# Performance work log

Hardware: AMD Instinct MI355X
Metric: run time of the kernel (lower is better)

Reference implementation:

```python
import jax, jax.numpy as jnp
import numpy as np

H = 16          # num_heads
EPS = 1e-5      # torch LayerNorm default eps


def setup_inputs() -> dict:
    key = jax.random.key(0)
    ks = jax.random.split(key, 12)
    B, S, D = 4, 2048, 1024
    sc = 1.0 / np.sqrt(D)
    return {
        "queries": jax.random.normal(ks[0], (B, S, D), jnp.float32),
        "keys": jax.random.normal(ks[1], (B, S, D), jnp.float32),
        "values": jax.random.normal(ks[2], (B, S, D), jnp.float32),
        "attention_mask": jax.random.randint(ks[3], (B, S), 0, 2, jnp.int32),
        "Wq": jax.random.normal(ks[4], (D, D), jnp.float32) * sc,
        "bq": jnp.zeros((D,), jnp.float32),
        "Wk": jax.random.normal(ks[5], (D, D), jnp.float32) * sc,
        "bk": jnp.zeros((D,), jnp.float32),
        "Wv": jax.random.normal(ks[6], (D, D), jnp.float32) * sc,
        "bv": jnp.zeros((D,), jnp.float32),
        "gamma": jnp.ones((D,), jnp.float32),
        "beta": jnp.zeros((D,), jnp.float32),
    }


def reference(queries, keys, values, attention_mask, Wq, bq, Wk, bk, Wv, bv, gamma, beta):
    B, S, D = queries.shape
    dh = D // H

    # QKV projections with ReLU epilogue (nn.Sequential(Linear, ReLU))
    q = jax.nn.relu(jnp.einsum("bsd,de->bse", queries, Wq) + bq)
    k = jax.nn.relu(jnp.einsum("bsd,de->bse", keys, Wk) + bk)
    v = jax.nn.relu(jnp.einsum("bsd,de->bse", values, Wv) + bv)

    # chunk along last dim + stack at dim=1  ==  [B,S,H,dh] -> [B,H,S,dh]
    q_ = q.reshape(B, S, H, dh).transpose(0, 2, 1, 3)
    k_ = k.reshape(B, S, H, dh).transpose(0, 2, 1, 3)
    v_ = v.reshape(B, S, H, dh).transpose(0, 2, 1, 3)

    # scaled dot-product scores [B,H,S,S]
    scores = jnp.einsum("bhqd,bhkd->bhqk", q_, k_) / jnp.sqrt(jnp.float32(dh))

    # mask[b,h,i,j] = attention_mask[b,i]; masked positions set to 1e-9
    # (faithful to torch.masked_fill(value=1e-09) in the original)
    m = attention_mask[:, None, :, None].astype(bool)  # [B,1,S,1]
    scores = jnp.where(m, scores, jnp.float32(1e-9))

    a = jax.nn.softmax(scores, axis=-1)
    o = jnp.einsum("bhqk,bhkd->bhqd", a, v_)          # [B,H,S,dh]
    o = o.transpose(0, 2, 1, 3).reshape(B, S, D)

    # residual + LayerNorm
    x = o + queries
    mu = jnp.mean(x, axis=-1, keepdims=True)
    var = jnp.mean(jnp.square(x - mu), axis=-1, keepdims=True)
    return (x - mu) * jax.lax.rsqrt(var + EPS) * gamma + beta
```

## Files before the change

kernel.cpp:

```cpp
#include <hip/hip_runtime.h>
#include <hip/hip_bf16.h>
#include <stdint.h>

typedef __bf16 bf16x8 __attribute__((ext_vector_type(8)));
typedef float f32x4 __attribute__((ext_vector_type(4)));
typedef float f32x16 __attribute__((ext_vector_type(16)));
typedef unsigned short ushort8v __attribute__((ext_vector_type(8)));
typedef unsigned short ushort4v __attribute__((ext_vector_type(4)));
typedef uint32_t uint2v __attribute__((ext_vector_type(2)));

#define MFMA16(a, b, c) __builtin_amdgcn_mfma_f32_16x16x32_bf16(a, b, c, 0, 0, 0)
#define MFMA32(a, b, c) __builtin_amdgcn_mfma_f32_32x32x16_bf16(a, b, c, 0, 0, 0)

#define GLOAD_LDS16(g, l)                                                        \
    __builtin_amdgcn_global_load_lds(                                            \
        (const __attribute__((address_space(1))) uint32_t*)(g),                  \
        (__attribute__((address_space(3))) uint32_t*)(l), 16, 0, 0)

__device__ __forceinline__ unsigned short f2bf_u(float f) {
    union { float f; uint32_t u; } cv; cv.f = f;
    uint32_t u = cv.u;
    uint32_t r = (u + 0x7FFFu + ((u >> 16) & 1u)) >> 16;
    return (unsigned short)r;
}

__device__ __forceinline__ uint32_t pkbf(float a, float b) {
    union { __hip_bfloat162 h; uint32_t u; } cv;
    cv.h = __float22bfloat162_rn(make_float2(a, b));
    return cv.u;
}

__device__ __forceinline__ float fexp2(float x) { return __builtin_amdgcn_exp2f(x); }

__global__ __launch_bounds__(256) void wt_cast(const float* __restrict__ W0,
                                               const float* __restrict__ W1,
                                               const float* __restrict__ W2,
                                               unsigned short* __restrict__ T0,
                                               unsigned short* __restrict__ T1,
                                               unsigned short* __restrict__ T2) {
    const int z = blockIdx.z;
    const float* W = z == 0 ? W0 : (z == 1 ? W1 : W2);
    unsigned short* Wt = z == 0 ? T0 : (z == 1 ? T1 : T2);
    __shared__ float t[32][33];
    const int tx = threadIdx.x & 31, ty = threadIdx.x >> 5;
    const int n0 = blockIdx.x * 32, k0 = blockIdx.y * 32;
#pragma unroll
    for (int i = 0; i < 4; i++) {
        int r = i * 8 + ty;
        t[r][tx] = W[(size_t)(k0 + r) * 1024 + n0 + tx];
    }
    __syncthreads();
#pragma unroll
    for (int i = 0; i < 4; i++) {
        int r = i * 8 + ty;
        Wt[(size_t)(n0 + r) * 1024 + k0 + tx] = f2bf_u(t[tx][r]);
    }
}

__global__ __launch_bounds__(256) void qkv_gemm2(
    const float* __restrict__ Aq, const float* __restrict__ Ak, const float* __restrict__ Av,
    const unsigned short* __restrict__ Wq, const unsigned short* __restrict__ Wk,
    const unsigned short* __restrict__ Wv,
    const float* __restrict__ biasq, const float* __restrict__ biask,
    const float* __restrict__ biasv,
    unsigned short* __restrict__ outq, unsigned short* __restrict__ outk,
    unsigned short* __restrict__ outv) {
    __shared__ __align__(16) unsigned short aS[2][128 * 32];
    __shared__ __align__(16) unsigned short wS[2][128 * 32];
    const int id = blockIdx.x;
    const int xcd = id & 7;
    const int local = id >> 3;
    const int z = local >> 6;
    const int l2i = local & 63;
    const int m0 = (xcd * 8 + (l2i >> 3)) * 128;
    const int n0 = (l2i & 7) * 128;

    const float* A = z == 0 ? Aq : (z == 1 ? Ak : Av);
    const unsigned short* Wt = z == 0 ? Wq : (z == 1 ? Wk : Wv);
    const float* bias = z == 0 ? biasq : (z == 1 ? biask : biasv);
    unsigned short* out = z == 0 ? outq : (z == 1 ? outk : outv);
    const bool vt = (z == 2);

    const int tid = threadIdx.x;
    const int lane = tid & 63, wave = tid >> 6;
    const int rrow = lane & 15, rgrp = lane >> 4;
    const int wm = wave >> 1, wn = wave & 1;

    const int wrow0 = tid >> 2, wc0 = tid & 3;
    const int wrow1 = (tid + 256) >> 2;
    const int arow_f = wm * 64 + rrow;
    const int brow_f = wn * 64 + rrow;

    f32x4 acc[4][4];
#pragma unroll
    for (int i = 0; i < 4; i++)
#pragma unroll
        for (int j = 0; j < 4; j++) acc[i][j] = (f32x4)0.0f;

    auto STAGE_W = [&](int k0, int bufi) {
        const char* src = (const char*)Wt;
        char* dst = (char*)&wS[bufi][0] + wave * 1024;
        GLOAD_LDS16(src + ((size_t)(n0 + wrow0) * 1024 + k0 + wc0 * 8) * 2, dst);
        GLOAD_LDS16(src + ((size_t)(n0 + wrow1) * 1024 + k0 + wc0 * 8) * 2, dst + 4096);
    };
    auto LOAD_A = [&](int k0, float4* r) {
#pragma unroll
        for (int i = 0; i < 4; i++) {
            const int g = i * 256 + tid, row = g >> 3, qc = g & 7;
            r[i] = *reinterpret_cast<const float4*>(A + (size_t)(m0 + row) * 1024 + k0 + qc * 4);
        }
    };
    auto WRITE_A = [&](const float4* r, int bufi) {
#pragma unroll
        for (int i = 0; i < 4; i++) {
            const int g = i * 256 + tid, row = g >> 3, qc = g & 7;
            uint2v w;
            w[0] = pkbf(r[i].x, r[i].y);
            w[1] = pkbf(r[i].z, r[i].w);
            *reinterpret_cast<uint2v*>((char*)&aS[bufi][0] + row * 64 + qc * 8) = w;
        }
    };

    {
        float4 a0[4];
        STAGE_W(0, 0);
        LOAD_A(0, a0);
        WRITE_A(a0, 0);
    }
    __syncthreads();

    for (int ks = 0; ks < 32; ks++) {
        const int cur = ks & 1;
        float4 anx[4];
        if (ks < 31) {
            STAGE_W((ks + 1) * 32, cur ^ 1);
            LOAD_A((ks + 1) * 32, anx);
        }

        bf16x8 af[4], bfr[4];
#pragma unroll
        for (int mi = 0; mi < 4; mi++)
            af[mi] = *reinterpret_cast<const bf16x8*>(
                (const char*)&aS[cur][0] + (arow_f + mi * 16) * 64 + rgrp * 16);
#pragma unroll
        for (int ni = 0; ni < 4; ni++)
            bfr[ni] = *reinterpret_cast<const bf16x8*>(
                (const char*)&wS[cur][0] + (brow_f + ni * 16) * 64 + rgrp * 16);
        __builtin_amdgcn_s_setprio(1);
#pragma unroll
        for (int mi = 0; mi < 4; mi++)
#pragma unroll
            for (int ni = 0; ni < 4; ni++)
                acc[mi][ni] = MFMA16(af[mi], bfr[ni], acc[mi][ni]);
        __builtin_amdgcn_s_setprio(0);

        if (ks < 31) WRITE_A(anx, cur ^ 1);
        __syncthreads();
    }

#pragma unroll
    for (int mi = 0; mi < 4; mi++) {
#pragma unroll
        for (int ni = 0; ni < 4; ni++) {
            const int n = n0 + wn * 64 + ni * 16 + rrow;
            const float bv = bias[n];
            const int h = n >> 6, d = n & 63;
            const int mbase = m0 + wm * 64 + mi * 16 + rgrp * 4;
            const int b = mbase >> 11, s = mbase & 2047;
            if (vt) {
                ushort4v pv;
#pragma unroll
                for (int jr = 0; jr < 4; jr++)
                    pv[jr] = f2bf_u(fmaxf(acc[mi][ni][jr] + bv, 0.0f));
                *reinterpret_cast<ushort4v*>(out + ((size_t)((b * 16 + h) * 64 + d)) * 2048 + s) = pv;
            } else {
#pragma unroll
                for (int jr = 0; jr < 4; jr++)
                    out[((size_t)((b * 16 + h) * 2048 + (s + jr))) * 64 + d] =
                        f2bf_u(fmaxf(acc[mi][ni][jr] + bv, 0.0f));
            }
        }
    }
}

__global__ __launch_bounds__(256, 4) void flash_attn(const unsigned short* __restrict__ Qg,
                                                     const unsigned short* __restrict__ Kg,
                                                     const unsigned short* __restrict__ Vt,
                                                     const int* __restrict__ mask,
                                                     float* __restrict__ O) {
    __shared__ __align__(16) unsigned short ldsK[2][64 * 64];
    __shared__ __align__(16) unsigned short ldsV[2][64 * 64];
    const int tid = threadIdx.x;
    const int lane = tid & 63, wave = tid >> 6;
    const int c = lane & 31, hi = lane >> 5;
    const int bid = blockIdx.x;
    const int swzb = (bid & 7) * 128 + (bid >> 3);
    const int gid = swzb * 4 + wave;
    const int bh = gid >> 6;
    const int q0 = (gid & 63) * 32;
    const int b = bh >> 4, h = bh & 15;
    const size_t base = (size_t)bh * (2048 * 64);
    const unsigned short* Qb = Qg + base;
    const unsigned short* Kb = Kg + base;
    const unsigned short* Vb = Vt + base;

    const int srow = lane >> 3;
    const int schunk = (lane & 7) ^ srow;
    int offL[4], offH[4];
#pragma unroll
    for (int ds = 0; ds < 4; ds++) {
        offL[ds] = c * 128 + ((((ds << 1) + hi) ^ (c & 7)) << 4);
        offH[ds] = offL[ds] + 32 * 128;
    }

    bf16x8 qf[4];
#pragma unroll
    for (int ds = 0; ds < 4; ds++)
        qf[ds] = *reinterpret_cast<const bf16x8*>(Qb + (size_t)(q0 + c) * 64 + ds * 16 + hi * 8);

    const int mk = mask[b * 2048 + q0 + c];
    const float sc = mk ? 0.1803368801f : 0.0f;

    union { uint32_t u[4]; bf16x8 v; } onesf;
#pragma unroll
    for (int i = 0; i < 4; i++) onesf.u[i] = 0x3F803F80u;

    f32x16 lacc = (f32x16)0.0f;
    f32x16 oacc0 = (f32x16)0.0f, oacc1 = (f32x16)0.0f;

    auto STAGE = [&](int kt, int bufi) {
        const char* ktile = (const char*)Kb + (size_t)kt * 8192;
        const char* vtile = (const char*)Vb + (size_t)kt * 128;
        char* kdst = (char*)&ldsK[bufi][0] + wave * 2048;
        char* vdst = (char*)&ldsV[bufi][0] + wave * 2048;
#pragma unroll
        for (int i = 0; i < 2; i++) {
            const int row = wave * 16 + i * 8 + srow;
            GLOAD_LDS16(ktile + row * 128 + schunk * 16, kdst + i * 1024);
            GLOAD_LDS16(vtile + (size_t)row * 4096 + schunk * 16, vdst + i * 1024);
        }
    };

    STAGE(0, 0);
    __syncthreads();

    for (int kt = 0; kt < 32; kt++) {
        const int cur = kt & 1;
        if (kt < 31) STAGE(kt + 1, cur ^ 1);
        const char* kbuf = (const char*)&ldsK[cur][0];
        const char* vbuf = (const char*)&ldsV[cur][0];

        f32x16 sacc0 = (f32x16)0.0f, sacc1 = (f32x16)0.0f;
        __builtin_amdgcn_s_setprio(1);
#pragma unroll
        for (int ds = 0; ds < 4; ds++) {
            bf16x8 k0 = *reinterpret_cast<const bf16x8*>(kbuf + offL[ds]);
            bf16x8 k1 = *reinterpret_cast<const bf16x8*>(kbuf + offH[ds]);
            sacc0 = MFMA32(k0, qf[ds], sacc0);
            sacc1 = MFMA32(k1, qf[ds], sacc1);
        }
        __builtin_amdgcn_s_setprio(0);

#pragma unroll
        for (int j = 0; j < 16; j++) {
            sacc0[j] = fexp2(sacc0[j] * sc);
            sacc1[j] = fexp2(sacc1[j] * sc);
        }

        {
            uint32_t w0[8];
#pragma unroll
            for (int i = 0; i < 8; i++) w0[i] = pkbf(sacc0[2 * i], sacc0[2 * i + 1]);
            uint32_t s00 = __shfl_xor(hi ? w0[0] : w0[2], 32, 64);
            uint32_t s01 = __shfl_xor(hi ? w0[1] : w0[3], 32, 64);
            uint32_t s02 = __shfl_xor(hi ? w0[4] : w0[6], 32, 64);
            uint32_t s03 = __shfl_xor(hi ? w0[5] : w0[7], 32, 64);
            union { uint32_t u[4]; bf16x8 v; } pa[2];
            if (hi == 0) {
                pa[0].u[0] = w0[0]; pa[0].u[1] = w0[1]; pa[0].u[2] = s00; pa[0].u[3] = s01;
                pa[1].u[0] = w0[4]; pa[1].u[1] = w0[5]; pa[1].u[2] = s02; pa[1].u[3] = s03;
            } else {
                pa[0].u[0] = s00; pa[0].u[1] = s01; pa[0].u[2] = w0[2]; pa[0].u[3] = w0[3];
                pa[1].u[0] = s02; pa[1].u[1] = s03; pa[1].u[2] = w0[6]; pa[1].u[3] = w0[7];
            }
            __builtin_amdgcn_s_setprio(1);
#pragma unroll
            for (int ks = 0; ks < 2; ks++) {
                bf16x8 v0 = *reinterpret_cast<const bf16x8*>(vbuf + offL[ks]);
                bf16x8 v1 = *reinterpret_cast<const bf16x8*>(vbuf + offH[ks]);
                lacc = MFMA32(pa[ks].v, onesf.v, lacc);
                oacc0 = MFMA32(pa[ks].v, v0, oacc0);
                oacc1 = MFMA32(pa[ks].v, v1, oacc1);
            }
            __builtin_amdgcn_s_setprio(0);
        }
        {
            uint32_t w1[8];
#pragma unroll
            for (int i = 0; i < 8; i++) w1[i] = pkbf(sacc1[2 * i], sacc1[2 * i + 1]);
            uint32_t s10 = __shfl_xor(hi ? w1[0] : w1[2], 32, 64);
            uint32_t s11 = __shfl_xor(hi ? w1[1] : w1[3], 32, 64);
            uint32_t s12 = __shfl_xor(hi ? w1[4] : w1[6], 32, 64);
            uint32_t s13 = __shfl_xor(hi ? w1[5] : w1[7], 32, 64);
            union { uint32_t u[4]; bf16x8 v; } pa[2];
            if (hi == 0) {
                pa[0].u[0] = w1[0]; pa[0].u[1] = w1[1]; pa[0].u[2] = s10; pa[0].u[3] = s11;
                pa[1].u[0] = w1[4]; pa[1].u[1] = w1[5]; pa[1].u[2] = s12; pa[1].u[3] = s13;
            } else {
                pa[0].u[0] = s10; pa[0].u[1] = s11; pa[0].u[2] = w1[2]; pa[0].u[3] = w1[3];
                pa[1].u[0] = s12; pa[1].u[1] = s13; pa[1].u[2] = w1[6]; pa[1].u[3] = w1[7];
            }
            __builtin_amdgcn_s_setprio(1);
#pragma unroll
            for (int ks = 0; ks < 2; ks++) {
                bf16x8 v0 = *reinterpret_cast<const bf16x8*>(vbuf + offL[2 + ks]);
                bf16x8 v1 = *reinterpret_cast<const bf16x8*>(vbuf + offH[2 + ks]);
                lacc = MFMA32(pa[ks].v, onesf.v, lacc);
                oacc0 = MFMA32(pa[ks].v, v0, oacc0);
                oacc1 = MFMA32(pa[ks].v, v1, oacc1);
            }
            __builtin_amdgcn_s_setprio(0);
        }

        __syncthreads();
    }

#pragma unroll
    for (int reg = 0; reg < 16; reg++) {
        const int rr = (reg & 3) + 8 * (reg >> 2) + 4 * hi;
        const float ir = 1.0f / lacc[reg];
        const size_t rowoff = (size_t)(b * 2048 + q0 + rr) * 1024 + h * 64 + c;
        O[rowoff]      = oacc0[reg] * ir;
        O[rowoff + 32] = oacc1[reg] * ir;
    }
}

__global__ __launch_bounds__(256) void resid_ln(const float* __restrict__ O,
                                                const float* __restrict__ Qin,
                                                const float* __restrict__ gamma,
                                                const float* __restrict__ beta,
                                                float* __restrict__ out) {
    __shared__ float red[4];
    const int row = blockIdx.x, tid = threadIdx.x;
    const size_t base = (size_t)row * 1024 + tid * 4;
    float4 o4 = *reinterpret_cast<const float4*>(O + base);
    float4 q4 = *reinterpret_cast<const float4*>(Qin + base);
    float x0 = o4.x + q4.x, x1 = o4.y + q4.y, x2 = o4.z + q4.z, x3 = o4.w + q4.w;

    float s = x0 + x1 + x2 + x3;
#pragma unroll
    for (int off = 32; off >= 1; off >>= 1) s += __shfl_xor(s, off, 64);
    const int w = tid >> 6;
    if ((tid & 63) == 0) red[w] = s;
    __syncthreads();
    const float mean = (red[0] + red[1] + red[2] + red[3]) * (1.0f / 1024.0f);
    __syncthreads();

    const float d0 = x0 - mean, d1 = x1 - mean, d2 = x2 - mean, d3 = x3 - mean;
    float vs = d0 * d0 + d1 * d1 + d2 * d2 + d3 * d3;
#pragma unroll
    for (int off = 32; off >= 1; off >>= 1) vs += __shfl_xor(vs, off, 64);
    if ((tid & 63) == 0) red[w] = vs;
    __syncthreads();
    const float var = (red[0] + red[1] + red[2] + red[3]) * (1.0f / 1024.0f);
    const float rstd = rsqrtf(var + 1e-5f);

    float4 g = *reinterpret_cast<const float4*>(gamma + tid * 4);
    float4 be = *reinterpret_cast<const float4*>(beta + tid * 4);
    float4 r;
    r.x = d0 * rstd * g.x + be.x;
    r.y = d1 * rstd * g.y + be.y;
    r.z = d2 * rstd * g.z + be.z;
    r.w = d3 * rstd * g.w + be.w;
    *reinterpret_cast<float4*>(out + base) = r;
}

extern "C" void kernel_launch(void* const* d_in, const int* in_sizes, int n_in,
                              void* d_out, int out_size, void* d_ws, size_t ws_size,
                              hipStream_t stream) {
    const float* q_in = (const float*)d_in[0];
    const float* k_in = (const float*)d_in[1];
    const float* v_in = (const float*)d_in[2];
    const int* mask = (const int*)d_in[3];
    const float* Wq = (const float*)d_in[4];
    const float* bq = (const float*)d_in[5];
    const float* Wk = (const float*)d_in[6];
    const float* bk = (const float*)d_in[7];
    const float* Wv = (const float*)d_in[8];
    const float* bv = (const float*)d_in[9];
    const float* gamma = (const float*)d_in[10];
    const float* beta = (const float*)d_in[11];
    float* out = (float*)d_out;

    unsigned short* wtq = (unsigned short*)d_ws;
    unsigned short* wtk = wtq + 1024 * 1024;
    unsigned short* wtv = wtk + 1024 * 1024;
    unsigned short* Qb = wtv + 1024 * 1024;
    unsigned short* Kb = Qb + 8192 * 1024;
    unsigned short* Vtb = Kb + 8192 * 1024;
    float* Obuf = (float*)(Vtb + 8192 * 1024);

    dim3 tb(256);
    wt_cast<<<dim3(32, 32, 3), tb, 0, stream>>>(Wq, Wk, Wv, wtq, wtk, wtv);
    qkv_gemm2<<<dim3(1536), tb, 0, stream>>>(q_in, k_in, v_in, wtq, wtk, wtv,
                                             bq, bk, bv, Qb, Kb, Vtb);
    flash_attn<<<dim3(1024), tb, 0, stream>>>(Qb, Kb, Vtb, mask, Obuf);
    resid_ln<<<dim3(8192), tb, 0, stream>>>(Obuf, q_in, gamma, beta, out);
}
```

Baseline: 205.4 us.

## Pre-cast activations to bf16 and stage GEMM A tiles via direct LDS loads

Adds a separate kernel that converts the fp32 query/key/value activations to bf16 in workspace. The QKV GEMM then stages both A and W tiles with asynchronous global-to-LDS loads instead of loading fp32 into registers, converting, and writing to LDS. This removes per-iteration VALU conversion and register staging from the GEMM main loop. In exchange it adds an extra kernel launch and a full extra read/write pass over the activations, and reuses the cast buffer for the attention output.

```diff
diff --git a/kernel.cpp b/kernel.cpp
--- a/kernel.cpp
+++ b/kernel.cpp
@@ -7,7 +7,7 @@
 typedef float f32x16 __attribute__((ext_vector_type(16)));
 typedef unsigned short ushort8v __attribute__((ext_vector_type(8)));
 typedef unsigned short ushort4v __attribute__((ext_vector_type(4)));
-typedef uint32_t uint2v __attribute__((ext_vector_type(2)));
+typedef uint32_t uint4v __attribute__((ext_vector_type(4)));
 
 #define MFMA16(a, b, c) __builtin_amdgcn_mfma_f32_16x16x32_bf16(a, b, c, 0, 0, 0)
 #define MFMA32(a, b, c) __builtin_amdgcn_mfma_f32_32x32x16_bf16(a, b, c, 0, 0, 0)
@@ -57,8 +57,29 @@
     }
 }
 
-__global__ __launch_bounds__(256) void qkv_gemm2(
-    const float* __restrict__ Aq, const float* __restrict__ Ak, const float* __restrict__ Av,
+__global__ __launch_bounds__(256) void acast(const float* __restrict__ A0,
+                                             const float* __restrict__ A1,
+                                             const float* __restrict__ A2,
+                                             unsigned short* __restrict__ B0,
+                                             unsigned short* __restrict__ B1,
+                                             unsigned short* __restrict__ B2) {
+    const int z = blockIdx.y;
+    const float* A = z == 0 ? A0 : (z == 1 ? A1 : A2);
+    unsigned short* B = z == 0 ? B0 : (z == 1 ? B1 : B2);
+    const size_t i = ((size_t)blockIdx.x * 256 + threadIdx.x) * 8;
+    const float4 f0 = *reinterpret_cast<const float4*>(A + i);
+    const float4 f1 = *reinterpret_cast<const float4*>(A + i + 4);
+    uint4v u;
+    u[0] = pkbf(f0.x, f0.y);
+    u[1] = pkbf(f0.z, f0.w);
+    u[2] = pkbf(f1.x, f1.y);
+    u[3] = pkbf(f1.z, f1.w);
+    *reinterpret_cast<uint4v*>(B + i) = u;
+}
+
+__global__ __launch_bounds__(256) void qkv_gemm3(
+    const unsigned short* __restrict__ Aq, const unsigned short* __restrict__ Ak,
+    const unsigned short* __restrict__ Av,
     const unsigned short* __restrict__ Wq, const unsigned short* __restrict__ Wk,
     const unsigned short* __restrict__ Wv,
     const float* __restrict__ biasq, const float* __restrict__ biask,
@@ -75,7 +96,7 @@
     const int m0 = (xcd * 8 + (l2i >> 3)) * 128;
     const int n0 = (l2i & 7) * 128;
 
-    const float* A = z == 0 ? Aq : (z == 1 ? Ak : Av);
+    const unsigned short* A = z == 0 ? Aq : (z == 1 ? Ak : Av);
     const unsigned short* Wt = z == 0 ? Wq : (z == 1 ? Wk : Wv);
     const float* bias = z == 0 ? biasq : (z == 1 ? biask : biasv);
     unsigned short* out = z == 0 ? outq : (z == 1 ? outk : outv);
@@ -86,8 +107,8 @@
     const int rrow = lane & 15, rgrp = lane >> 4;
     const int wm = wave >> 1, wn = wave & 1;
 
-    const int wrow0 = tid >> 2, wc0 = tid & 3;
-    const int wrow1 = (tid + 256) >> 2;
+    const int row0 = tid >> 2, c0 = tid & 3;
+    const int row1 = (tid + 256) >> 2;
     const int arow_f = wm * 64 + rrow;
     const int brow_f = wn * 64 + rrow;
 
@@ -97,44 +118,22 @@
 #pragma unroll
         for (int j = 0; j < 4; j++) acc[i][j] = (f32x4)0.0f;
 
-    auto STAGE_W = [&](int k0, int bufi) {
-        const char* src = (const char*)Wt;
-        char* dst = (char*)&wS[bufi][0] + wave * 1024;
-        GLOAD_LDS16(src + ((size_t)(n0 + wrow0) * 1024 + k0 + wc0 * 8) * 2, dst);
-        GLOAD_LDS16(src + ((size_t)(n0 + wrow1) * 1024 + k0 + wc0 * 8) * 2, dst + 4096);
+    auto STAGE = [&](const unsigned short* src, int r0, int k0, void* dstbase) {
+        char* dst = (char*)dstbase + wave * 1024;
+        GLOAD_LDS16((const char*)src + ((size_t)(r0 + row0) * 1024 + k0 + c0 * 8) * 2, dst);
+        GLOAD_LDS16((const char*)src + ((size_t)(r0 + row1) * 1024 + k0 + c0 * 8) * 2,
+                    dst + 4096);
     };
-    auto LOAD_A = [&](int k0, float4* r) {
-#pragma unroll
-        for (int i = 0; i < 4; i++) {
-            const int g = i * 256 + tid, row = g >> 3, qc = g & 7;
-            r[i] = *reinterpret_cast<const float4*>(A + (size_t)(m0 + row) * 1024 + k0 + qc * 4);
-        }
-    };
-    auto WRITE_A = [&](const float4* r, int bufi) {
-#pragma unroll
-        for (int i = 0; i < 4; i++) {
-            const int g = i * 256 + tid, row = g >> 3, qc = g & 7;
-            uint2v w;
-            w[0] = pkbf(r[i].x, r[i].y);
-            w[1] = pkbf(r[i].z, r[i].w);
-            *reinterpret_cast<uint2v*>((char*)&aS[bufi][0] + row * 64 + qc * 8) = w;
-        }
-    };
-
-    {
-        float4 a0[4];
-        STAGE_W(0, 0);
-        LOAD_A(0, a0);
-        WRITE_A(a0, 0);
-    }
+
+    STAGE(A, m0, 0, &aS[0][0]);
+    STAGE(Wt, n0, 0, &wS[0][0]);
     __syncthreads();
 
     for (int ks = 0; ks < 32; ks++) {
         const int cur = ks & 1;
-        float4 anx[4];
         if (ks < 31) {
-            STAGE_W((ks + 1) * 32, cur ^ 1);
-            LOAD_A((ks + 1) * 32, anx);
+            STAGE(A, m0, (ks + 1) * 32, &aS[cur ^ 1][0]);
+            STAGE(Wt, n0, (ks + 1) * 32, &wS[cur ^ 1][0]);
         }
 
         bf16x8 af[4], bfr[4];
@@ -154,7 +153,6 @@
                 acc[mi][ni] = MFMA16(af[mi], bfr[ni], acc[mi][ni]);
         __builtin_amdgcn_s_setprio(0);
 
-        if (ks < 31) WRITE_A(anx, cur ^ 1);
         __syncthreads();
     }
 
@@ -398,11 +396,15 @@
     unsigned short* Qb = wtv + 1024 * 1024;
     unsigned short* Kb = Qb + 8192 * 1024;
     unsigned short* Vtb = Kb + 8192 * 1024;
-    float* Obuf = (float*)(Vtb + 8192 * 1024);
+    unsigned short* Aqb = Vtb + 8192 * 1024;
+    unsigned short* Akb = Aqb + 8192 * 1024;
+    unsigned short* Avb = Akb + 8192 * 1024;
+    float* Obuf = (float*)Aqb;
 
     dim3 tb(256);
     wt_cast<<<dim3(32, 32, 3), tb, 0, stream>>>(Wq, Wk, Wv, wtq, wtk, wtv);
-    qkv_gemm2<<<dim3(1536), tb, 0, stream>>>(q_in, k_in, v_in, wtq, wtk, wtv,
+    acast<<<dim3(4096, 3), tb, 0, stream>>>(q_in, k_in, v_in, Aqb, Akb, Avb);
+    qkv_gemm3<<<dim3(1536), tb, 0, stream>>>(Aqb, Akb, Avb, wtq, wtk, wtv,
                                              bq, bk, bv, Qb, Kb, Vtb);
     flash_attn<<<dim3(1024), tb, 0, stream>>>(Qb, Kb, Vtb, mask, Obuf);
     resid_ln<<<dim3(8192), tb, 0, stream>>>(Obuf, q_in, gamma, beta, out);
```

After: 206.9 us. Within noise of the previous version (+0.7%).
